# Kernel tuning notes

Hardware: AMD Instinct MI355X
Metric: run time of the kernel (lower is better)

Reference implementation:

```python
import jax, jax.numpy as jnp
import numpy as np

D_MODEL = 2048
NUM_HEADS = 32
NUM_KV_HEADS = 8
HEAD_DIM = D_MODEL // NUM_HEADS  # 64
KV_DIM = NUM_KV_HEADS * HEAD_DIM  # 512


def setup_inputs() -> dict:
    key = jax.random.key(0)
    ks = jax.random.split(key, 9)
    s = 1.0 / np.sqrt(D_MODEL)
    x = jax.random.normal(ks[0], (4, 1024, D_MODEL), dtype=jnp.float32)
    Wq = jax.random.uniform(ks[1], (D_MODEL, D_MODEL), jnp.float32, -s, s)
    bq = jax.random.uniform(ks[2], (D_MODEL,), jnp.float32, -s, s)
    Wk = jax.random.uniform(ks[3], (D_MODEL, KV_DIM), jnp.float32, -s, s)
    bk = jax.random.uniform(ks[4], (KV_DIM,), jnp.float32, -s, s)
    Wv = jax.random.uniform(ks[5], (D_MODEL, KV_DIM), jnp.float32, -s, s)
    bv = jax.random.uniform(ks[6], (KV_DIM,), jnp.float32, -s, s)
    Wo = jax.random.uniform(ks[7], (D_MODEL, D_MODEL), jnp.float32, -s, s)
    bo = jax.random.uniform(ks[8], (D_MODEL,), jnp.float32, -s, s)
    return {"x": x, "Wq": Wq, "bq": bq, "Wk": Wk, "bk": bk,
            "Wv": Wv, "bv": bv, "Wo": Wo, "bo": bo}


def reference(x, Wq, bq, Wk, bk, Wv, bv, Wo, bo):
    B, S, _ = x.shape
    g = NUM_HEADS // NUM_KV_HEADS  # heads per kv head
    # projections
    q = (x @ Wq + bq).reshape(B, S, NUM_HEADS, HEAD_DIM).transpose(0, 2, 1, 3)   # [B,H,S,d]
    k = (x @ Wk + bk).reshape(B, S, NUM_KV_HEADS, HEAD_DIM).transpose(0, 2, 1, 3)  # [B,Hkv,S,d]
    v = (x @ Wv + bv).reshape(B, S, NUM_KV_HEADS, HEAD_DIM).transpose(0, 2, 1, 3)
    # repeat_interleave KV heads across query-head groups
    k = jnp.repeat(k, g, axis=1)  # [B,H,S,d]
    v = jnp.repeat(v, g, axis=1)
    scores = jnp.einsum('bhqd,bhkd->bhqk', q, k) / np.sqrt(HEAD_DIM)  # [B,H,S,S]
    attn = jax.nn.softmax(scores, axis=-1)
    ctx = jnp.einsum('bhqk,bhkd->bhqd', attn, v)  # [B,H,S,d]
    ctx = ctx.transpose(0, 2, 1, 3).reshape(B, S, D_MODEL)
    return ctx @ Wo + bo
```

## Files before the change

### kernel.cpp

```cpp
#include <hip/hip_runtime.h>
#include <stdint.h>

typedef unsigned short u16;
typedef __attribute__((ext_vector_type(8))) __bf16 bf16x8;
typedef __attribute__((ext_vector_type(4))) __bf16 bf16x4;
typedef __attribute__((ext_vector_type(4))) float f32x4;
typedef __attribute__((ext_vector_type(16))) float f32x16;

#define QSCALE 0.1803368801111204f

#if __has_builtin(__builtin_amdgcn_exp2f)
#define EXP2(x) __builtin_amdgcn_exp2f(x)
#else
#define EXP2(x) exp2f(x)
#endif

__device__ __forceinline__ u16 f2bf(float f) {
  uint32_t u = __float_as_uint(f);
  u += 0x7fffu + ((u >> 16) & 1u);
  return (u16)(u >> 16);
}
__device__ __forceinline__ float bf2f(u16 h) {
  return __uint_as_float(((uint32_t)h) << 16);
}
__device__ __forceinline__ uint32_t pack2bf(float a, float b) {
  return (uint32_t)f2bf(a) | ((uint32_t)f2bf(b) << 16);
}

__device__ __forceinline__ void gl_lds16(const u16* g, u16* l) {
  __builtin_amdgcn_global_load_lds(
      (const __attribute__((address_space(1))) unsigned int*)g,
      (__attribute__((address_space(3))) unsigned int*)l, 16, 0, 0);
}

__device__ __forceinline__ uint32_t cvt_pk_bf16(float lo, float hi) {
  uint32_t r;
  asm("v_cvt_pk_bf16_f32 %0, %1, %2" : "=v"(r) : "v"(lo), "v"(hi));
  return r;
}
__device__ __forceinline__ void pl32_swap(uint32_t& x, uint32_t& y) {
  asm("v_permlane32_swap_b32 %0, %1" : "+v"(x), "+v"(y));
}

#define S_BAR() __builtin_amdgcn_s_barrier()
#define LGKM0() do { __asm__ volatile("s_waitcnt lgkmcnt(0)" ::: "memory"); \
                     __builtin_amdgcn_sched_barrier(0); } while (0)
#define VMC(N) do { __asm__ volatile("s_waitcnt vmcnt(" #N ")" ::: "memory"); \
                    __builtin_amdgcn_sched_barrier(0); } while (0)

__global__ void detect_dtype(const u16* __restrict__ x, int* __restrict__ flag) {
  __shared__ int any_huge;
  if (threadIdx.x == 0) any_huge = 0;
  __syncthreads();
  int huge = 0;
  for (int i = threadIdx.x; i < 4096; i += 256) {
    float v = bf2f(x[i]);
    if (!(fabsf(v) < 1e6f)) huge = 1;
  }
  if (huge) any_huge = 1;
  __syncthreads();
  if (threadIdx.x == 0) *flag = any_huge;
}

__global__ __launch_bounds__(256) void prep(
    const void* __restrict__ Wq, const void* __restrict__ Wk,
    const void* __restrict__ Wv, const void* __restrict__ Wo,
    const void* __restrict__ x,
    const void* __restrict__ bq, const void* __restrict__ bk,
    const void* __restrict__ bv, const void* __restrict__ bo,
    u16* __restrict__ WT, u16* __restrict__ WoT, u16* __restrict__ xb,
    float* __restrict__ biasf, const int* __restrict__ flag) {
  const int fl = *flag;
  int id = blockIdx.x;
  const int tid = threadIdx.x;
  if (id < 2560) {
    __shared__ u16 tile[64 * 72];
    const void* in; u16* outp; int N, rowoff;
    if (id < 1024)      { in = Wq; outp = WT;  N = 2048; rowoff = 0; }
    else if (id < 1280) { in = Wk; outp = WT;  N = 512;  rowoff = 2048; id -= 1024; }
    else if (id < 1536) { in = Wv; outp = WT;  N = 512;  rowoff = 2560; id -= 1280; }
    else                { in = Wo; outp = WoT; N = 2048; rowoff = 0;    id -= 1536; }
    int tiles_x = N >> 6;
    int nb = (id % tiles_x) * 64, kb = (id / tiles_x) * 64;
    const int kbase = (tid >> 4) * 4, nc = (tid & 15) * 4;
    if (fl) {
      float4 L[4];
#pragma unroll
      for (int p = 0; p < 4; ++p)
        L[p] = *(const float4*)&((const float*)in)[(size_t)(kb + kbase + p) * N + nb + nc];
#pragma unroll
      for (int nj = 0; nj < 4; ++nj) {
        uint2 w;
        w.x = pack2bf(((const float*)&L[0])[nj], ((const float*)&L[1])[nj]);
        w.y = pack2bf(((const float*)&L[2])[nj], ((const float*)&L[3])[nj]);
        *(uint2*)&tile[(nc + nj) * 72 + kbase] = w;
      }
    } else {
      uint2 L[4];
#pragma unroll
      for (int p = 0; p < 4; ++p)
        L[p] = *(const uint2*)&((const u16*)in)[(size_t)(kb + kbase + p) * N + nb + nc];
#pragma unroll
      for (int nj = 0; nj < 4; ++nj) {
        uint2 w;
        w.x = (uint32_t)((const u16*)&L[0])[nj] | ((uint32_t)((const u16*)&L[1])[nj] << 16);
        w.y = (uint32_t)((const u16*)&L[2])[nj] | ((uint32_t)((const u16*)&L[3])[nj] << 16);
        *(uint2*)&tile[(nc + nj) * 72 + kbase] = w;
      }
    }
    __syncthreads();
#pragma unroll
    for (int it = 0; it < 2; ++it) {
      int sid = it * 256 + tid;
      int row = sid >> 3, kseg = (sid & 7) * 8;
      uint4 v = *(const uint4*)&tile[row * 72 + kseg];
      *(uint4*)&outp[(size_t)(rowoff + nb + row) * 2048 + kb + kseg] = v;
    }
  } else if (id < 4608) {
    size_t base = ((size_t)(id - 2560) * 256 + tid) * 16;
    if (fl) {
      const float* xf = (const float*)x;
      float4 a = *(const float4*)&xf[base];
      float4 b = *(const float4*)&xf[base + 4];
      float4 c = *(const float4*)&xf[base + 8];
      float4 d = *(const float4*)&xf[base + 12];
      uint4 o0, o1;
      o0.x = pack2bf(a.x, a.y); o0.y = pack2bf(a.z, a.w);
      o0.z = pack2bf(b.x, b.y); o0.w = pack2bf(b.z, b.w);
      o1.x = pack2bf(c.x, c.y); o1.y = pack2bf(c.z, c.w);
      o1.z = pack2bf(d.x, d.y); o1.w = pack2bf(d.z, d.w);
      *(uint4*)&xb[base] = o0;
      *(uint4*)&xb[base + 8] = o1;
    } else {
      const u16* x16 = (const u16*)x;
      *(uint4*)&xb[base] = *(const uint4*)&x16[base];
      *(uint4*)&xb[base + 8] = *(const uint4*)&x16[base + 8];
    }
  } else {
    int i = (id - 4608) * 256 + tid;
    if (i < 5120) {
      const void* src; int idx;
      if (i < 2048)      { src = bq; idx = i; }
      else if (i < 2560) { src = bk; idx = i - 2048; }
      else if (i < 3072) { src = bv; idx = i - 2560; }
      else               { src = bo; idx = i - 3072; }
      biasf[i] = fl ? ((const float*)src)[idx] : bf2f(((const u16*)src)[idx]);
    }
  }
}

__global__ __launch_bounds__(512, 2) void gemm_qkv(
    const u16* __restrict__ A, const u16* __restrict__ BT,
    const float* __restrict__ bias,
    u16* __restrict__ qo, u16* __restrict__ ko, u16* __restrict__ vo) {
  __shared__ __align__(16) u16 lds[65536];
  const int tid = threadIdx.x;
  const int wave = tid >> 6, lane = tid & 63;
  const int ln = lane & 15, quad = lane >> 4;
  const int sw8 = 8 * (quad ^ ((ln >> 1) & 3));
  const int m0 = blockIdx.y * 128, n0 = blockIdx.x * 384;

  u16* const A0b = lds;
  u16* const A1b = lds + 8192;
  u16* const B0b = lds + 16384;
  u16* const B1b = lds + 40960;

  const int srow = wave * 16 + (lane >> 2);
  const int skq = 8 * ((lane & 3) ^ ((lane >> 3) & 3));
  const u16* const sa = A + (size_t)(m0 + srow) * 2048 + skq;
  const u16* const sb = BT + (size_t)(n0 + srow) * 2048 + skq;
  const int dc8 = (wave * 64 + lane) * 8;

  auto stageA = [&](u16* dbase, int kt) {
    const u16* s = sa + kt;
    gl_lds16(s, dbase + dc8);
    gl_lds16(s + 32, dbase + dc8 + 4096);
  };
  auto stageB = [&](u16* dbase, int u, int kt) {
    const u16* s = sb + (size_t)u * 262144 + kt;
    u16* d = dbase + u * 4096 + dc8;
    gl_lds16(s, d);
    gl_lds16(s + 32, d + 12288);
  };

  f32x4 acc[8][3];
#pragma unroll
  for (int i = 0; i < 8; ++i)
#pragma unroll
    for (int j = 0; j < 3; ++j) acc[i][j] = {0.f, 0.f, 0.f, 0.f};

  bf16x8 aL[8], aH[8], b0f[2], b1f[2], b2f[2];
  auto rdAh = [&](bf16x8* dst, const u16* buf, int ibase) {
#pragma unroll
    for (int ii = 0; ii < 4; ++ii) {
      const int ro = ((ibase + ii) * 16 + ln) * 32 + sw8;
      dst[ii * 2 + 0] = *(const bf16x8*)&buf[ro];
      dst[ii * 2 + 1] = *(const bf16x8*)&buf[ro + 4096];
    }
  };
  auto rdBj = [&](bf16x8* dst, const u16* buf, int j) {
    const int ro = (wave * 48 + j * 16 + ln) * 32 + sw8;
    dst[0] = *(const bf16x8*)&buf[ro];
    dst[1] = *(const bf16x8*)&buf[ro + 12288];
  };
  auto mma8 = [&](const bf16x8* a4, const bf16x8* bj, int ibase, int j) {
#pragma unroll
    for (int ii = 0; ii < 4; ++ii)
#pragma unroll
      for (int kh = 0; kh < 2; ++kh)
        acc[ibase + ii][j] = __builtin_amdgcn_mfma_f32_16x16x32_bf16(
            bj[kh], a4[ii * 2 + kh], acc[ibase + ii][j], 0, 0, 0);
  };

  stageA(A0b, 0);
  stageB(B0b, 0, 0); stageB(B0b, 1, 0); stageB(B0b, 2, 0);
  stageA(A1b, 64);
  __asm__ volatile("s_waitcnt vmcnt(2)" ::: "memory");
  S_BAR();

#pragma unroll 1
  for (int it = 0; it < 16; ++it) {
    const int kk = it * 128;
#pragma unroll
    for (int h = 0; h < 2; ++h) {
      u16* const Ab = h ? A1b : A0b;
      u16* const Bb = h ? B1b : B0b;
      u16* const Bo = h ? B0b : B1b;
      const int kB = (kk + 64 + h * 64) & 2047;
      const int kA = (kk + 128 + h * 64) & 2047;
      rdAh(aL, Ab, 0); rdBj(b0f, Bb, 0);
      stageB(Bo, 0, kB);
      S_BAR(); LGKM0();
      __builtin_amdgcn_s_setprio(1); mma8(aL, b0f, 0, 0); __builtin_amdgcn_s_setprio(0);
      S_BAR();
      rdAh(aH, Ab, 4); rdBj(b1f, Bb, 1);
      stageB(Bo, 1, kB);
      S_BAR(); LGKM0();
      __builtin_amdgcn_s_setprio(1); mma8(aH, b0f, 4, 0); mma8(aL, b1f, 0, 1); __builtin_amdgcn_s_setprio(0);
      S_BAR();
      rdBj(b2f, Bb, 2);
      stageB(Bo, 2, kB);
      S_BAR(); LGKM0();
      __builtin_amdgcn_s_setprio(1); mma8(aH, b1f, 4, 1); mma8(aL, b2f, 0, 2); __builtin_amdgcn_s_setprio(0);
      S_BAR();
      stageA(Ab, kA);
      S_BAR();
      __builtin_amdgcn_s_setprio(1); mma8(aH, b2f, 4, 2); __builtin_amdgcn_s_setprio(0);
      VMC(2);
      S_BAR();
    }
  }

#pragma unroll
  for (int j = 0; j < 3; ++j) {
    const int gnf = n0 + wave * 48 + j * 16;
    const int gn = gnf + quad * 4;
    const float4 bsv = *(const float4*)&bias[gn];
    if (gnf < 2048) {
      const int hh = gn >> 6, dd = gn & 63;
#pragma unroll
      for (int i = 0; i < 8; ++i) {
        const int m = m0 + i * 16 + ln;
        const int b = m >> 10, s = m & 1023;
        uint2 st;
        st.x = pack2bf((acc[i][j][0] + bsv.x) * QSCALE, (acc[i][j][1] + bsv.y) * QSCALE);
        st.y = pack2bf((acc[i][j][2] + bsv.z) * QSCALE, (acc[i][j][3] + bsv.w) * QSCALE);
        *(uint2*)&qo[(((size_t)(b * 32 + hh)) * 1024 + s) * 64 + dd] = st;
      }
    } else if (gnf < 2560) {
      const int n2 = gn - 2048, hh = n2 >> 6, dd = n2 & 63;
#pragma unroll
      for (int i = 0; i < 8; ++i) {
        const int m = m0 + i * 16 + ln;
        const int b = m >> 10, s = m & 1023;
        uint2 st;
        st.x = pack2bf(acc[i][j][0] + bsv.x, acc[i][j][1] + bsv.y);
        st.y = pack2bf(acc[i][j][2] + bsv.z, acc[i][j][3] + bsv.w);
        *(uint2*)&ko[(((size_t)(b * 8 + hh)) * 1024 + s) * 64 + dd] = st;
      }
    } else {
      const int n2 = gn - 2560, hh = n2 >> 6, dd0 = n2 & 63;
#pragma unroll
      for (int i = 0; i < 8; ++i) {
        const int m = m0 + i * 16 + ln;
        const int b = m >> 10, s = m & 1023;
        const size_t vb = ((size_t)(b * 8 + hh) * 64 + dd0) * 1024 + s;
        vo[vb]        = f2bf(acc[i][j][0] + bsv.x);
        vo[vb + 1024] = f2bf(acc[i][j][1] + bsv.y);
        vo[vb + 2048] = f2bf(acc[i][j][2] + bsv.z);
        vo[vb + 3072] = f2bf(acc[i][j][3] + bsv.w);
      }
    }
  }
}

__global__ __launch_bounds__(512, 2) void gemm_o(
    const u16* __restrict__ A, const u16* __restrict__ BT,
    const float* __restrict__ bias, u16* __restrict__ o0,
    const int* __restrict__ flag) {
  __shared__ __align__(16) u16 lds[49152];
  const int tid = threadIdx.x;
  const int wave = tid >> 6, lane = tid & 63;
  const int ln = lane & 15, quad = lane >> 4;
  const int sw8 = 8 * (quad ^ ((ln >> 1) & 3));
  const int wm = (wave >> 2) * 128, wn = (wave & 3) * 32;
  const int m0 = blockIdx.y * 256, n0 = blockIdx.x * 128;
  const int fl = *flag;

  u16* const A0b = lds;
  u16* const A1b = lds + 16384;
  u16* const B0b = lds + 32768;
  u16* const B1b = lds + 40960;

  const int srow = wave * 16 + (lane >> 2);
  const int skq = 8 * ((lane & 3) ^ ((lane >> 3) & 3));
  const u16* const sa = A + (size_t)(m0 + srow) * 2048 + skq;
  const u16* const sb = BT + (size_t)(n0 + srow) * 2048 + skq;
  const int dc8 = (wave * 64 + lane) * 8;

  auto stageA = [&](u16* dbase, int H, int kt) {
    const u16* s = sa + (size_t)H * 262144 + kt;
    u16* d = dbase + H * 4096 + dc8;
    gl_lds16(s, d);
    gl_lds16(s + 32, d + 8192);
  };
  auto stageB = [&](u16* dbase, int kt) {
    const u16* s = sb + kt;
    gl_lds16(s, dbase + dc8);
    gl_lds16(s + 32, dbase + dc8 + 4096);
  };

  f32x4 acc[8][2];
#pragma unroll
  for (int i = 0; i < 8; ++i)
#pragma unroll
    for (int j = 0; j < 2; ++j) acc[i][j] = {0.f, 0.f, 0.f, 0.f};

  bf16x8 aL[8], aH[8], b0f[2], b1f[2];
  auto rdAh = [&](bf16x8* dst, const u16* buf, int ibase) {
#pragma unroll
    for (int ii = 0; ii < 4; ++ii) {
      const int ro = (wm + (ibase + ii) * 16 + ln) * 32 + sw8;
      dst[ii * 2 + 0] = *(const bf16x8*)&buf[ro];
      dst[ii * 2 + 1] = *(const bf16x8*)&buf[ro + 8192];
    }
  };
  auto rdBj = [&](bf16x8* dst, const u16* buf, int j) {
    const int ro = (wn + j * 16 + ln) * 32 + sw8;
    dst[0] = *(const bf16x8*)&buf[ro];
    dst[1] = *(const bf16x8*)&buf[ro + 4096];
  };
  auto mma8 = [&](const bf16x8* a4, const bf16x8* bj, int ibase, int j) {
#pragma unroll
    for (int ii = 0; ii < 4; ++ii)
#pragma unroll
      for (int kh = 0; kh < 2; ++kh)
        acc[ibase + ii][j] = __builtin_amdgcn_mfma_f32_16x16x32_bf16(
            bj[kh], a4[ii * 2 + kh], acc[ibase + ii][j], 0, 0, 0);
  };

  stageA(A0b, 0, 0); stageA(A0b, 1, 0);
  stageB(B0b, 0);
  stageA(A1b, 0, 64); stageA(A1b, 1, 64);
  __asm__ volatile("s_waitcnt vmcnt(4)" ::: "memory");
  S_BAR();

#pragma unroll 1
  for (int it = 0; it < 16; ++it) {
    const int kk = it * 128;
#pragma unroll
    for (int h = 0; h < 2; ++h) {
      u16* const Ab = h ? A1b : A0b;
      u16* const Bb = h ? B1b : B0b;
      u16* const Bo = h ? B0b : B1b;
      const int kB = (kk + 64 + h * 64) & 2047;
      const int kA = (kk + 128 + h * 64) & 2047;
      rdAh(aL, Ab, 0); rdBj(b0f, Bb, 0);
      stageB(Bo, kB);
      S_BAR(); LGKM0();
      __builtin_amdgcn_s_setprio(1); mma8(aL, b0f, 0, 0); __builtin_amdgcn_s_setprio(0);
      S_BAR();
      rdAh(aH, Ab, 4); rdBj(b1f, Bb, 1);
      S_BAR(); LGKM0();
      __builtin_amdgcn_s_setprio(1); mma8(aH, b0f, 4, 0); __builtin_amdgcn_s_setprio(0);
      S_BAR();
      stageA(Ab, 0, kA);
      S_BAR();
      __builtin_amdgcn_s_setprio(1); mma8(aH, b1f, 4, 1); __builtin_amdgcn_s_setprio(0);
      S_BAR();
      stageA(Ab, 1, kA);
      S_BAR();
      __builtin_amdgcn_s_setprio(1); mma8(aL, b1f, 0, 1); __builtin_amdgcn_s_setprio(0);
      VMC(4);
      S_BAR();
    }
  }

#pragma unroll
  for (int j = 0; j < 2; ++j) {
    const int nbase = n0 + wn + j * 16 + quad * 4;
    const float4 bsv = *(const float4*)&bias[nbase];
#pragma unroll
    for (int i = 0; i < 8; ++i) {
      const int m = m0 + wm + i * 16 + ln;
      float v0 = acc[i][j][0] + bsv.x, v1 = acc[i][j][1] + bsv.y;
      float v2 = acc[i][j][2] + bsv.z, v3 = acc[i][j][3] + bsv.w;
      if (fl) {
        float4 st = {v0, v1, v2, v3};
        *(float4*)&((float*)o0)[(size_t)m * 2048 + nbase] = st;
      } else {
        uint2 st; st.x = pack2bf(v0, v1); st.y = pack2bf(v2, v3);
        *(uint2*)&o0[(size_t)m * 2048 + nbase] = st;
      }
    }
  }
}

__global__ __launch_bounds__(256, 4) void attn_kernel(
    const u16* __restrict__ q_ws, const u16* __restrict__ k_ws,
    const u16* __restrict__ vt_ws, u16* __restrict__ ctx) {
  __shared__ __align__(16) u16 lds[16384];
  const int tid = threadIdx.x;
  const int wave = tid >> 6, lane = tid & 63;
  const int l31 = lane & 31, hi = lane >> 5;
  const int sw = (l31 >> 1) & 3;
  const int qt = blockIdx.x, bh = blockIdx.y;
  const int b = bh >> 5, h = bh & 31, kvh = h >> 2;
  const int q0 = qt * 128 + wave * 32;
  const u16* const kptr = k_ws + (size_t)(b * 8 + kvh) * 65536;
  const u16* const vptr = vt_ws + (size_t)(b * 8 + kvh) * 65536;

  bf16x8 qf[4];
  {
    const size_t qb = (size_t)bh * 65536 + (size_t)(q0 + l31) * 64 + hi * 8;
#pragma unroll
    for (int ck = 0; ck < 4; ++ck) qf[ck] = *(const bf16x8*)&q_ws[qb + ck * 16];
  }

  const int strow = tid >> 2;
  const int stq = (tid & 3) ^ ((strow >> 1) & 3);
  const u16* const ks = kptr + strow * 64 + stq * 8;
  const u16* const vs = vptr + strow * 1024 + stq * 8;
  u16* const kd = &lds[tid * 8];
  u16* const vd = &lds[8192 + tid * 8];

  auto stageK = [&](int buf, int tile) {
    const u16* s = ks + tile * 4096;
    gl_lds16(s, kd + buf * 4096);
    gl_lds16(s + 32, kd + buf * 4096 + 2048);
  };
  auto stageV = [&](int buf, int tile) {
    const u16* s = vs + tile * 64;
    gl_lds16(s, vd + buf * 4096);
    gl_lds16(s + 32, vd + buf * 4096 + 2048);
  };

  f32x16 oacc0, oacc1;
#pragma unroll
  for (int r = 0; r < 16; ++r) { oacc0[r] = 0.f; oacc1[r] = 0.f; }
  float lsum = 0.f;

  auto qk = [&](int kh, int buf) -> f32x16 {
    f32x16 s;
#pragma unroll
    for (int r = 0; r < 16; ++r) s[r] = 0.f;
#pragma unroll
    for (int ck = 0; ck < 4; ++ck) {
      const int dq = (((ck & 1) << 1) | hi) ^ sw;
      bf16x8 kf = *(const bf16x8*)&lds[buf * 4096 + kh * 1024 + (ck >> 1) * 2048 +
                                       l31 * 32 + dq * 8];
      s = __builtin_amdgcn_mfma_f32_32x32x16_bf16(kf, qf[ck], s, 0, 0, 0);
    }
    return s;
  };

  auto softmax = [&](const f32x16& s, uint32_t* w) {
    float p[16];
#pragma unroll
    for (int r = 0; r < 16; ++r) p[r] = EXP2(s[r]);
    float t0 = (p[0] + p[1]) + (p[2] + p[3]);
    float t1 = (p[4] + p[5]) + (p[6] + p[7]);
    float t2 = (p[8] + p[9]) + (p[10] + p[11]);
    float t3 = (p[12] + p[13]) + (p[14] + p[15]);
    lsum += (t0 + t1) + (t2 + t3);
#pragma unroll
    for (int a = 0; a < 4; ++a) {
      w[a * 2 + 0] = cvt_pk_bf16(p[4 * a + 0], p[4 * a + 1]);
      w[a * 2 + 1] = cvt_pk_bf16(p[4 * a + 2], p[4 * a + 3]);
    }
  };

  auto pv = [&](uint32_t* w, int mm, int kh, int buf) {
    uint32_t x0 = w[4 * mm + 0], y0 = w[4 * mm + 2];
    uint32_t x1 = w[4 * mm + 1], y1 = w[4 * mm + 3];
    pl32_swap(x0, y0);
    pl32_swap(x1, y1);
    union { uint32_t u[4]; bf16x8 v; } pu;
    pu.u[0] = x0; pu.u[1] = x1; pu.u[2] = y0; pu.u[3] = y1;
    const int m = kh * 2 + mm;
    const int sq = ((((m & 1) << 1) | hi) ^ sw);
    const int vbase = 8192 + buf * 4096 + (m >> 1) * 2048 + l31 * 32 + sq * 8;
    bf16x8 vf0 = *(const bf16x8*)&lds[vbase];
    bf16x8 vf1 = *(const bf16x8*)&lds[vbase + 1024];
    oacc0 = __builtin_amdgcn_mfma_f32_32x32x16_bf16(pu.v, vf0, oacc0, 0, 0, 0);
    oacc1 = __builtin_amdgcn_mfma_f32_32x32x16_bf16(pu.v, vf1, oacc1, 0, 0, 0);
  };

  stageK(0, 0); stageV(0, 0);
  stageK(1, 1); stageV(1, 1);
  VMC(4);
  S_BAR();

#pragma unroll 1
  for (int it = 0; it < 16; ++it) {
    const int c = it & 1;
    f32x16 s0 = qk(0, c);
    uint32_t w0[8];
    softmax(s0, w0);
    pv(w0, 0, 0, c); pv(w0, 1, 0, c);
    f32x16 s1 = qk(1, c);
    uint32_t w1[8];
    softmax(s1, w1);
    pv(w1, 0, 1, c); pv(w1, 1, 1, c);
    if (it < 15) S_BAR();
    if (it < 14) {
      stageK(c, it + 2); stageV(c, it + 2);
      VMC(4);
      S_BAR();
    } else if (it == 14) {
      VMC(0);
      S_BAR();
    }
  }

  float lt = lsum + __shfl_xor(lsum, 32);
  const float inv = 1.0f / lt;
  const int ha = hi << 4;
  const size_t cb = (size_t)(b * 1024) * 2048 + (size_t)h * 64;
#pragma unroll
  for (int r = 0; r < 16; ++r) {
    const int qr = (r & 3) + 8 * (r >> 2);
    float iq = __uint_as_float(
        (uint32_t)__builtin_amdgcn_ds_bpermute(qr * 4 + ha, (int)__float_as_uint(inv)));
    const int q = q0 + qr + 4 * hi;
    const size_t rowb = cb + (size_t)q * 2048;
    ctx[rowb + l31]      = f2bf(oacc0[r] * iq);
    ctx[rowb + 32 + l31] = f2bf(oacc1[r] * iq);
  }
}

extern "C" void kernel_launch(void* const* d_in, const int* in_sizes, int n_in,
                              void* d_out, int out_size, void* d_ws, size_t ws_size,
                              hipStream_t stream) {
  const void* x  = d_in[0];
  const void* Wq = d_in[1];
  const void* bq = d_in[2];
  const void* Wk = d_in[3];
  const void* bk = d_in[4];
  const void* Wv = d_in[5];
  const void* bv = d_in[6];
  const void* Wo = d_in[7];
  const void* bo = d_in[8];
  char* ws = (char*)d_ws;

  u16* WT    = (u16*)(ws + 0);
  u16* WoT   = (u16*)(ws + 12582912);
  u16* q_ws  = (u16*)(ws + 20971520);
  u16* k_ws  = (u16*)(ws + 37748736);
  u16* vt_ws = (u16*)(ws + 41943040);
  u16* c_ws  = (u16*)(ws + 46137344);
  u16* xb    = (u16*)(ws + 62914560);
  float* biasf = (float*)(ws + 79691776);
  int* flag  = (int*)(ws + 79712256);

  detect_dtype<<<1, 256, 0, stream>>>((const u16*)x, flag);
  prep<<<4628, 256, 0, stream>>>(Wq, Wk, Wv, Wo, x, bq, bk, bv, bo,
                                 WT, WoT, xb, biasf, flag);

  gemm_qkv<<<dim3(8, 32), 512, 0, stream>>>(xb, WT, biasf, q_ws, k_ws, vt_ws);
  attn_kernel<<<dim3(8, 128), 256, 0, stream>>>(q_ws, k_ws, vt_ws, c_ws);
  gemm_o<<<dim3(16, 16), 512, 0, stream>>>(c_ws, WoT, biasf + 3072, (u16*)d_out, flag);
}
```

Before: 259.0 us.

## Reshape per-wave tiles in QKV and output GEMMs to square-ish 64x96/64x64

Changes the wave-level decomposition in both projection GEMMs: QKV waves now cover 64 rows x 96 cols (2x4 grid) instead of 128x48, and the output GEMM uses 64x64 per wave instead of 128x32. Each wave loads one A fragment set and reuses it across more B column tiles, which lowers LDS read traffic per MFMA. The inner schedule is rewritten so the B staging loads are grouped differently and LGKM waits are added before the later MFMA groups. This may change how well LDS reads overlap with MFMAs and how much register pressure there is at the current launch bounds.

```diff
diff --git a/kernel.cpp b/kernel.cpp
--- a/kernel.cpp
+++ b/kernel.cpp
@@ -158,6 +158,8 @@
   const int wave = tid >> 6, lane = tid & 63;
   const int ln = lane & 15, quad = lane >> 4;
   const int sw8 = 8 * (quad ^ ((ln >> 1) & 3));
+  const int wmv = (wave >> 2) * 64;
+  const int wnv = (wave & 3) * 96;
   const int m0 = blockIdx.y * 128, n0 = blockIdx.x * 384;
 
   u16* const A0b = lds;
@@ -183,33 +185,33 @@
     gl_lds16(s + 32, d + 12288);
   };
 
-  f32x4 acc[8][3];
-#pragma unroll
-  for (int i = 0; i < 8; ++i)
-#pragma unroll
-    for (int j = 0; j < 3; ++j) acc[i][j] = {0.f, 0.f, 0.f, 0.f};
-
-  bf16x8 aL[8], aH[8], b0f[2], b1f[2], b2f[2];
-  auto rdAh = [&](bf16x8* dst, const u16* buf, int ibase) {
-#pragma unroll
-    for (int ii = 0; ii < 4; ++ii) {
-      const int ro = ((ibase + ii) * 16 + ln) * 32 + sw8;
-      dst[ii * 2 + 0] = *(const bf16x8*)&buf[ro];
-      dst[ii * 2 + 1] = *(const bf16x8*)&buf[ro + 4096];
+  f32x4 acc[4][6];
+#pragma unroll
+  for (int i = 0; i < 4; ++i)
+#pragma unroll
+    for (int j = 0; j < 6; ++j) acc[i][j] = {0.f, 0.f, 0.f, 0.f};
+
+  bf16x8 aF[8], bx[2], by[2], bz[2];
+  auto rdA = [&](const u16* buf) {
+#pragma unroll
+    for (int i = 0; i < 4; ++i) {
+      const int ro = (wmv + i * 16 + ln) * 32 + sw8;
+      aF[i * 2 + 0] = *(const bf16x8*)&buf[ro];
+      aF[i * 2 + 1] = *(const bf16x8*)&buf[ro + 4096];
     }
   };
   auto rdBj = [&](bf16x8* dst, const u16* buf, int j) {
-    const int ro = (wave * 48 + j * 16 + ln) * 32 + sw8;
+    const int ro = (wnv + j * 16 + ln) * 32 + sw8;
     dst[0] = *(const bf16x8*)&buf[ro];
     dst[1] = *(const bf16x8*)&buf[ro + 12288];
   };
-  auto mma8 = [&](const bf16x8* a4, const bf16x8* bj, int ibase, int j) {
-#pragma unroll
-    for (int ii = 0; ii < 4; ++ii)
+  auto mmaJ = [&](const bf16x8* bj, int j) {
+#pragma unroll
+    for (int i = 0; i < 4; ++i)
 #pragma unroll
       for (int kh = 0; kh < 2; ++kh)
-        acc[ibase + ii][j] = __builtin_amdgcn_mfma_f32_16x16x32_bf16(
-            bj[kh], a4[ii * 2 + kh], acc[ibase + ii][j], 0, 0, 0);
+        acc[i][j] = __builtin_amdgcn_mfma_f32_16x16x32_bf16(
+            bj[kh], aF[i * 2 + kh], acc[i][j], 0, 0, 0);
   };
 
   stageA(A0b, 0);
@@ -228,39 +230,38 @@
       u16* const Bo = h ? B0b : B1b;
       const int kB = (kk + 64 + h * 64) & 2047;
       const int kA = (kk + 128 + h * 64) & 2047;
-      rdAh(aL, Ab, 0); rdBj(b0f, Bb, 0);
-      stageB(Bo, 0, kB);
-      S_BAR(); LGKM0();
-      __builtin_amdgcn_s_setprio(1); mma8(aL, b0f, 0, 0); __builtin_amdgcn_s_setprio(0);
-      S_BAR();
-      rdAh(aH, Ab, 4); rdBj(b1f, Bb, 1);
-      stageB(Bo, 1, kB);
-      S_BAR(); LGKM0();
-      __builtin_amdgcn_s_setprio(1); mma8(aH, b0f, 4, 0); mma8(aL, b1f, 0, 1); __builtin_amdgcn_s_setprio(0);
-      S_BAR();
-      rdBj(b2f, Bb, 2);
-      stageB(Bo, 2, kB);
-      S_BAR(); LGKM0();
-      __builtin_amdgcn_s_setprio(1); mma8(aH, b1f, 4, 1); mma8(aL, b2f, 0, 2); __builtin_amdgcn_s_setprio(0);
-      S_BAR();
+      rdA(Ab); rdBj(bx, Bb, 0);
+      stageB(Bo, 0, kB); stageB(Bo, 1, kB); stageB(Bo, 2, kB);
+      S_BAR(); LGKM0();
+      __builtin_amdgcn_s_setprio(1); mmaJ(bx, 0); __builtin_amdgcn_s_setprio(0);
+      S_BAR();
+      rdBj(by, Bb, 1); rdBj(bz, Bb, 2);
+      S_BAR(); LGKM0();
+      __builtin_amdgcn_s_setprio(1); mmaJ(by, 1); mmaJ(bz, 2); __builtin_amdgcn_s_setprio(0);
+      S_BAR();
+      rdBj(bx, Bb, 3); rdBj(by, Bb, 4);
+      S_BAR(); LGKM0();
+      __builtin_amdgcn_s_setprio(1); mmaJ(bx, 3); mmaJ(by, 4); __builtin_amdgcn_s_setprio(0);
+      S_BAR();
+      rdBj(bz, Bb, 5);
       stageA(Ab, kA);
-      S_BAR();
-      __builtin_amdgcn_s_setprio(1); mma8(aH, b2f, 4, 2); __builtin_amdgcn_s_setprio(0);
+      S_BAR(); LGKM0();
+      __builtin_amdgcn_s_setprio(1); mmaJ(bz, 5); __builtin_amdgcn_s_setprio(0);
       VMC(2);
       S_BAR();
     }
   }
 
 #pragma unroll
-  for (int j = 0; j < 3; ++j) {
-    const int gnf = n0 + wave * 48 + j * 16;
+  for (int j = 0; j < 6; ++j) {
+    const int gnf = n0 + wnv + j * 16;
     const int gn = gnf + quad * 4;
     const float4 bsv = *(const float4*)&bias[gn];
     if (gnf < 2048) {
       const int hh = gn >> 6, dd = gn & 63;
 #pragma unroll
-      for (int i = 0; i < 8; ++i) {
-        const int m = m0 + i * 16 + ln;
+      for (int i = 0; i < 4; ++i) {
+        const int m = m0 + wmv + i * 16 + ln;
         const int b = m >> 10, s = m & 1023;
         uint2 st;
         st.x = pack2bf((acc[i][j][0] + bsv.x) * QSCALE, (acc[i][j][1] + bsv.y) * QSCALE);
@@ -270,8 +271,8 @@
     } else if (gnf < 2560) {
       const int n2 = gn - 2048, hh = n2 >> 6, dd = n2 & 63;
 #pragma unroll
-      for (int i = 0; i < 8; ++i) {
-        const int m = m0 + i * 16 + ln;
+      for (int i = 0; i < 4; ++i) {
+        const int m = m0 + wmv + i * 16 + ln;
         const int b = m >> 10, s = m & 1023;
         uint2 st;
         st.x = pack2bf(acc[i][j][0] + bsv.x, acc[i][j][1] + bsv.y);
@@ -281,8 +282,8 @@
     } else {
       const int n2 = gn - 2560, hh = n2 >> 6, dd0 = n2 & 63;
 #pragma unroll
-      for (int i = 0; i < 8; ++i) {
-        const int m = m0 + i * 16 + ln;
+      for (int i = 0; i < 4; ++i) {
+        const int m = m0 + wmv + i * 16 + ln;
         const int b = m >> 10, s = m & 1023;
         const size_t vb = ((size_t)(b * 8 + hh) * 64 + dd0) * 1024 + s;
         vo[vb]        = f2bf(acc[i][j][0] + bsv.x);
@@ -303,7 +304,8 @@
   const int wave = tid >> 6, lane = tid & 63;
   const int ln = lane & 15, quad = lane >> 4;
   const int sw8 = 8 * (quad ^ ((ln >> 1) & 3));
-  const int wm = (wave >> 2) * 128, wn = (wave & 3) * 32;
+  const int wmv = (wave >> 1) * 64;
+  const int wnv = (wave & 1) * 64;
   const int m0 = blockIdx.y * 256, n0 = blockIdx.x * 128;
   const int fl = *flag;
 
@@ -330,33 +332,33 @@
     gl_lds16(s + 32, dbase + dc8 + 4096);
   };
 
-  f32x4 acc[8][2];
-#pragma unroll
-  for (int i = 0; i < 8; ++i)
-#pragma unroll
-    for (int j = 0; j < 2; ++j) acc[i][j] = {0.f, 0.f, 0.f, 0.f};
-
-  bf16x8 aL[8], aH[8], b0f[2], b1f[2];
-  auto rdAh = [&](bf16x8* dst, const u16* buf, int ibase) {
-#pragma unroll
-    for (int ii = 0; ii < 4; ++ii) {
-      const int ro = (wm + (ibase + ii) * 16 + ln) * 32 + sw8;
-      dst[ii * 2 + 0] = *(const bf16x8*)&buf[ro];
-      dst[ii * 2 + 1] = *(const bf16x8*)&buf[ro + 8192];
+  f32x4 acc[4][4];
+#pragma unroll
+  for (int i = 0; i < 4; ++i)
+#pragma unroll
+    for (int j = 0; j < 4; ++j) acc[i][j] = {0.f, 0.f, 0.f, 0.f};
+
+  bf16x8 aF[8], bx[2], by[2];
+  auto rdA = [&](const u16* buf) {
+#pragma unroll
+    for (int i = 0; i < 4; ++i) {
+      const int ro = (wmv + i * 16 + ln) * 32 + sw8;
+      aF[i * 2 + 0] = *(const bf16x8*)&buf[ro];
+      aF[i * 2 + 1] = *(const bf16x8*)&buf[ro + 8192];
     }
   };
   auto rdBj = [&](bf16x8* dst, const u16* buf, int j) {
-    const int ro = (wn + j * 16 + ln) * 32 + sw8;
+    const int ro = (wnv + j * 16 + ln) * 32 + sw8;
     dst[0] = *(const bf16x8*)&buf[ro];
     dst[1] = *(const bf16x8*)&buf[ro + 4096];
   };
-  auto mma8 = [&](const bf16x8* a4, const bf16x8* bj, int ibase, int j) {
-#pragma unroll
-    for (int ii = 0; ii < 4; ++ii)
+  auto mmaJ = [&](const bf16x8* bj, int j) {
+#pragma unroll
+    for (int i = 0; i < 4; ++i)
 #pragma unroll
       for (int kh = 0; kh < 2; ++kh)
-        acc[ibase + ii][j] = __builtin_amdgcn_mfma_f32_16x16x32_bf16(
-            bj[kh], a4[ii * 2 + kh], acc[ibase + ii][j], 0, 0, 0);
+        acc[i][j] = __builtin_amdgcn_mfma_f32_16x16x32_bf16(
+            bj[kh], aF[i * 2 + kh], acc[i][j], 0, 0, 0);
   };
 
   stageA(A0b, 0, 0); stageA(A0b, 1, 0);
@@ -375,34 +377,36 @@
       u16* const Bo = h ? B0b : B1b;
       const int kB = (kk + 64 + h * 64) & 2047;
       const int kA = (kk + 128 + h * 64) & 2047;
-      rdAh(aL, Ab, 0); rdBj(b0f, Bb, 0);
+      rdA(Ab); rdBj(bx, Bb, 0);
       stageB(Bo, kB);
       S_BAR(); LGKM0();
-      __builtin_amdgcn_s_setprio(1); mma8(aL, b0f, 0, 0); __builtin_amdgcn_s_setprio(0);
-      S_BAR();
-      rdAh(aH, Ab, 4); rdBj(b1f, Bb, 1);
-      S_BAR(); LGKM0();
-      __builtin_amdgcn_s_setprio(1); mma8(aH, b0f, 4, 0); __builtin_amdgcn_s_setprio(0);
-      S_BAR();
+      __builtin_amdgcn_s_setprio(1); mmaJ(bx, 0); __builtin_amdgcn_s_setprio(0);
+      S_BAR();
+      rdBj(by, Bb, 1);
+      S_BAR(); LGKM0();
+      __builtin_amdgcn_s_setprio(1); mmaJ(by, 1); __builtin_amdgcn_s_setprio(0);
+      S_BAR();
+      rdBj(bx, Bb, 2);
       stageA(Ab, 0, kA);
-      S_BAR();
-      __builtin_amdgcn_s_setprio(1); mma8(aH, b1f, 4, 1); __builtin_amdgcn_s_setprio(0);
-      S_BAR();
+      S_BAR(); LGKM0();
+      __builtin_amdgcn_s_setprio(1); mmaJ(bx, 2); __builtin_amdgcn_s_setprio(0);
+      S_BAR();
+      rdBj(by, Bb, 3);
       stageA(Ab, 1, kA);
-      S_BAR();
-      __builtin_amdgcn_s_setprio(1); mma8(aL, b1f, 0, 1); __builtin_amdgcn_s_setprio(0);
+      S_BAR(); LGKM0();
+      __builtin_amdgcn_s_setprio(1); mmaJ(by, 3); __builtin_amdgcn_s_setprio(0);
       VMC(4);
       S_BAR();
     }
   }
 
 #pragma unroll
-  for (int j = 0; j < 2; ++j) {
-    const int nbase = n0 + wn + j * 16 + quad * 4;
+  for (int j = 0; j < 4; ++j) {
+    const int nbase = n0 + wnv + j * 16 + quad * 4;
     const float4 bsv = *(const float4*)&bias[nbase];
 #pragma unroll
-    for (int i = 0; i < 8; ++i) {
-      const int m = m0 + wm + i * 16 + ln;
+    for (int i = 0; i < 4; ++i) {
+      const int m = m0 + wmv + i * 16 + ln;
       float v0 = acc[i][j][0] + bsv.x, v1 = acc[i][j][1] + bsv.y;
       float v2 = acc[i][j][2] + bsv.z, v3 = acc[i][j][3] + bsv.w;
       if (fl) {
```

New measurement: 269.5 us. 1.04x slower.

## Process two query sub-tiles per wave with 512-thread attention blocks

Applied to the files above, without the earlier changes.

The attention kernel now uses 512-thread blocks that each cover 512 query rows, and every wave handles 64 query rows as two 32-row sub-tiles. Each K/V fragment read from LDS feeds twice as many MFMAs, and each block stages K/V tiles for four times as many queries, so K/V global and LDS traffic per query drops. The cost is a 4x smaller grid (256 blocks), which may leave CUs underused on a 256-CU part, plus higher register pressure from four output accumulators.

```diff
diff --git a/kernel.cpp b/kernel.cpp
--- a/kernel.cpp
+++ b/kernel.cpp
@@ -416,7 +416,7 @@
   }
 }
 
-__global__ __launch_bounds__(256, 4) void attn_kernel(
+__global__ __launch_bounds__(512, 2) void attn_kernel(
     const u16* __restrict__ q_ws, const u16* __restrict__ k_ws,
     const u16* __restrict__ vt_ws, u16* __restrict__ ctx) {
   __shared__ __align__(16) u16 lds[16384];
@@ -426,58 +426,54 @@
   const int sw = (l31 >> 1) & 3;
   const int qt = blockIdx.x, bh = blockIdx.y;
   const int b = bh >> 5, h = bh & 31, kvh = h >> 2;
-  const int q0 = qt * 128 + wave * 32;
+  const int q0 = qt * 512 + wave * 64;
   const u16* const kptr = k_ws + (size_t)(b * 8 + kvh) * 65536;
   const u16* const vptr = vt_ws + (size_t)(b * 8 + kvh) * 65536;
 
-  bf16x8 qf[4];
+  bf16x8 qfA[4], qfB[4];
   {
-    const size_t qb = (size_t)bh * 65536 + (size_t)(q0 + l31) * 64 + hi * 8;
-#pragma unroll
-    for (int ck = 0; ck < 4; ++ck) qf[ck] = *(const bf16x8*)&q_ws[qb + ck * 16];
-  }
-
-  const int strow = tid >> 2;
-  const int stq = (tid & 3) ^ ((strow >> 1) & 3);
-  const u16* const ks = kptr + strow * 64 + stq * 8;
-  const u16* const vs = vptr + strow * 1024 + stq * 8;
+    const size_t qa = (size_t)bh * 65536 + (size_t)(q0 + l31) * 64 + hi * 8;
+    const size_t qb = qa + (size_t)32 * 64;
+#pragma unroll
+    for (int ck = 0; ck < 4; ++ck) {
+      qfA[ck] = *(const bf16x8*)&q_ws[qa + ck * 16];
+      qfB[ck] = *(const bf16x8*)&q_ws[qb + ck * 16];
+    }
+  }
+
+  const int r = (tid >> 2) & 63;
+  const int sq8 = 8 * ((tid & 3) ^ ((r >> 1) & 3));
+  const int koff = (tid >> 8) * 32;
+  const u16* const ks = kptr + r * 64 + koff + sq8;
+  const u16* const vs = vptr + r * 1024 + koff + sq8;
   u16* const kd = &lds[tid * 8];
   u16* const vd = &lds[8192 + tid * 8];
 
-  auto stageK = [&](int buf, int tile) {
-    const u16* s = ks + tile * 4096;
-    gl_lds16(s, kd + buf * 4096);
-    gl_lds16(s + 32, kd + buf * 4096 + 2048);
-  };
-  auto stageV = [&](int buf, int tile) {
-    const u16* s = vs + tile * 64;
-    gl_lds16(s, vd + buf * 4096);
-    gl_lds16(s + 32, vd + buf * 4096 + 2048);
-  };
-
-  f32x16 oacc0, oacc1;
-#pragma unroll
-  for (int r = 0; r < 16; ++r) { oacc0[r] = 0.f; oacc1[r] = 0.f; }
-  float lsum = 0.f;
-
-  auto qk = [&](int kh, int buf) -> f32x16 {
-    f32x16 s;
-#pragma unroll
-    for (int r = 0; r < 16; ++r) s[r] = 0.f;
+  auto stageK = [&](int buf, int tile) { gl_lds16(ks + tile * 4096, kd + buf * 4096); };
+  auto stageV = [&](int buf, int tile) { gl_lds16(vs + tile * 64, vd + buf * 4096); };
+
+  f32x16 oA0, oA1, oB0, oB1;
+#pragma unroll
+  for (int rr = 0; rr < 16; ++rr) { oA0[rr] = 0.f; oA1[rr] = 0.f; oB0[rr] = 0.f; oB1[rr] = 0.f; }
+  float lsA = 0.f, lsB = 0.f;
+
+  auto qk2 = [&](int kh, int buf, f32x16& sA, f32x16& sB) {
+#pragma unroll
+    for (int rr = 0; rr < 16; ++rr) { sA[rr] = 0.f; sB[rr] = 0.f; }
 #pragma unroll
     for (int ck = 0; ck < 4; ++ck) {
       const int dq = (((ck & 1) << 1) | hi) ^ sw;
       bf16x8 kf = *(const bf16x8*)&lds[buf * 4096 + kh * 1024 + (ck >> 1) * 2048 +
                                        l31 * 32 + dq * 8];
-      s = __builtin_amdgcn_mfma_f32_32x32x16_bf16(kf, qf[ck], s, 0, 0, 0);
-    }
-    return s;
-  };
-
-  auto softmax = [&](const f32x16& s, uint32_t* w) {
+      sA = __builtin_amdgcn_mfma_f32_32x32x16_bf16(kf, qfA[ck], sA, 0, 0, 0);
+      sB = __builtin_amdgcn_mfma_f32_32x32x16_bf16(kf, qfB[ck], sB, 0, 0, 0);
+    }
+  };
+
+  auto softmax = [&](const f32x16& s, uint32_t* w, float& lsum) {
     float p[16];
 #pragma unroll
-    for (int r = 0; r < 16; ++r) p[r] = EXP2(s[r]);
+    for (int rr = 0; rr < 16; ++rr) p[rr] = EXP2(s[rr]);
     float t0 = (p[0] + p[1]) + (p[2] + p[3]);
     float t1 = (p[4] + p[5]) + (p[6] + p[7]);
     float t2 = (p[8] + p[9]) + (p[10] + p[11]);
@@ -490,42 +486,51 @@
     }
   };
 
-  auto pv = [&](uint32_t* w, int mm, int kh, int buf) {
+  auto mkfrag = [&](uint32_t* w, int mm) -> bf16x8 {
     uint32_t x0 = w[4 * mm + 0], y0 = w[4 * mm + 2];
     uint32_t x1 = w[4 * mm + 1], y1 = w[4 * mm + 3];
     pl32_swap(x0, y0);
     pl32_swap(x1, y1);
     union { uint32_t u[4]; bf16x8 v; } pu;
     pu.u[0] = x0; pu.u[1] = x1; pu.u[2] = y0; pu.u[3] = y1;
+    return pu.v;
+  };
+
+  auto pv2 = [&](uint32_t* wA, uint32_t* wB, int mm, int kh, int buf) {
+    bf16x8 pA = mkfrag(wA, mm);
+    bf16x8 pB = mkfrag(wB, mm);
     const int m = kh * 2 + mm;
     const int sq = ((((m & 1) << 1) | hi) ^ sw);
     const int vbase = 8192 + buf * 4096 + (m >> 1) * 2048 + l31 * 32 + sq * 8;
     bf16x8 vf0 = *(const bf16x8*)&lds[vbase];
     bf16x8 vf1 = *(const bf16x8*)&lds[vbase + 1024];
-    oacc0 = __builtin_amdgcn_mfma_f32_32x32x16_bf16(pu.v, vf0, oacc0, 0, 0, 0);
-    oacc1 = __builtin_amdgcn_mfma_f32_32x32x16_bf16(pu.v, vf1, oacc1, 0, 0, 0);
+    oA0 = __builtin_amdgcn_mfma_f32_32x32x16_bf16(pA, vf0, oA0, 0, 0, 0);
+    oA1 = __builtin_amdgcn_mfma_f32_32x32x16_bf16(pA, vf1, oA1, 0, 0, 0);
+    oB0 = __builtin_amdgcn_mfma_f32_32x32x16_bf16(pB, vf0, oB0, 0, 0, 0);
+    oB1 = __builtin_amdgcn_mfma_f32_32x32x16_bf16(pB, vf1, oB1, 0, 0, 0);
   };
 
   stageK(0, 0); stageV(0, 0);
   stageK(1, 1); stageV(1, 1);
-  VMC(4);
+  VMC(2);
   S_BAR();
 
 #pragma unroll 1
   for (int it = 0; it < 16; ++it) {
     const int c = it & 1;
-    f32x16 s0 = qk(0, c);
-    uint32_t w0[8];
-    softmax(s0, w0);
-    pv(w0, 0, 0, c); pv(w0, 1, 0, c);
-    f32x16 s1 = qk(1, c);
-    uint32_t w1[8];
-    softmax(s1, w1);
-    pv(w1, 0, 1, c); pv(w1, 1, 1, c);
+    f32x16 sA, sB;
+    qk2(0, c, sA, sB);
+    uint32_t wA0[8], wB0[8];
+    softmax(sA, wA0, lsA); softmax(sB, wB0, lsB);
+    pv2(wA0, wB0, 0, 0, c); pv2(wA0, wB0, 1, 0, c);
+    qk2(1, c, sA, sB);
+    uint32_t wA1[8], wB1[8];
+    softmax(sA, wA1, lsA); softmax(sB, wB1, lsB);
+    pv2(wA1, wB1, 0, 1, c); pv2(wA1, wB1, 1, 1, c);
     if (it < 15) S_BAR();
     if (it < 14) {
       stageK(c, it + 2); stageV(c, it + 2);
-      VMC(4);
+      VMC(2);
       S_BAR();
     } else if (it == 14) {
       VMC(0);
@@ -533,19 +538,26 @@
     }
   }
 
-  float lt = lsum + __shfl_xor(lsum, 32);
-  const float inv = 1.0f / lt;
+  float ltA = lsA + __shfl_xor(lsA, 32);
+  float ltB = lsB + __shfl_xor(lsB, 32);
+  const float invA = 1.0f / ltA;
+  const float invB = 1.0f / ltB;
   const int ha = hi << 4;
   const size_t cb = (size_t)(b * 1024) * 2048 + (size_t)h * 64;
 #pragma unroll
-  for (int r = 0; r < 16; ++r) {
-    const int qr = (r & 3) + 8 * (r >> 2);
-    float iq = __uint_as_float(
-        (uint32_t)__builtin_amdgcn_ds_bpermute(qr * 4 + ha, (int)__float_as_uint(inv)));
-    const int q = q0 + qr + 4 * hi;
-    const size_t rowb = cb + (size_t)q * 2048;
-    ctx[rowb + l31]      = f2bf(oacc0[r] * iq);
-    ctx[rowb + 32 + l31] = f2bf(oacc1[r] * iq);
+  for (int rr = 0; rr < 16; ++rr) {
+    const int qr = (rr & 3) + 8 * (rr >> 2);
+    float iqA = __uint_as_float(
+        (uint32_t)__builtin_amdgcn_ds_bpermute(qr * 4 + ha, (int)__float_as_uint(invA)));
+    float iqB = __uint_as_float(
+        (uint32_t)__builtin_amdgcn_ds_bpermute(qr * 4 + ha, (int)__float_as_uint(invB)));
+    const int qA = q0 + qr + 4 * hi;
+    const size_t rowA = cb + (size_t)qA * 2048;
+    const size_t rowB = rowA + (size_t)32 * 2048;
+    ctx[rowA + l31]      = f2bf(oA0[rr] * iqA);
+    ctx[rowA + 32 + l31] = f2bf(oA1[rr] * iqA);
+    ctx[rowB + l31]      = f2bf(oB0[rr] * iqB);
+    ctx[rowB + 32 + l31] = f2bf(oB1[rr] * iqB);
   }
 }
 
@@ -578,6 +590,6 @@
                                  WT, WoT, xb, biasf, flag);
 
   gemm_qkv<<<dim3(8, 32), 512, 0, stream>>>(xb, WT, biasf, q_ws, k_ws, vt_ws);
-  attn_kernel<<<dim3(8, 128), 256, 0, stream>>>(q_ws, k_ws, vt_ws, c_ws);
+  attn_kernel<<<dim3(2, 128), 512, 0, stream>>>(q_ws, k_ws, vt_ws, c_ws);
   gemm_o<<<dim3(16, 16), 512, 0, stream>>>(c_ws, WoT, biasf + 3072, (u16*)d_out, flag);
 }
```

After: 255.1 us, median of 2. About the same (-1.5%).
